# Performance work log

Measured on AMD Instinct MI355X. Metric: run time of the kernel, lower is better.

## Reference

```python
import jax, jax.numpy as jnp
import numpy as np

N_NODES = 50000
N_EDGES = 800000
D = 128          # node_state_dim
H = 256          # edge hidden / message dim (= 2*D)
NH = 256         # node MLP hidden


def setup_inputs() -> dict:
    key = jax.random.key(0)
    ks = jax.random.split(key, 20)
    s = 0.05
    inp = {
        "node_states": jax.random.normal(ks[0], (N_NODES, D), jnp.float32),
        "edge_features": jax.random.normal(ks[1], (N_EDGES, 1), jnp.float32),
        "from_idx": jax.random.randint(ks[2], (N_EDGES,), 0, N_NODES, jnp.int32),
        "to_idx": jax.random.randint(ks[3], (N_EDGES,), 0, N_NODES, jnp.int32),
        # forward-direction message net: Linear(2D+1 -> H), ReLU, Linear(H -> H)
        "W1": jax.random.normal(ks[4], (2 * D + 1, H), jnp.float32) * s,
        "b1": jnp.zeros((H,), jnp.float32),
        "W2": jax.random.normal(ks[5], (H, H), jnp.float32) * s,
        "b2": jnp.zeros((H,), jnp.float32),
        # reverse-direction message net (separate params)
        "RW1": jax.random.normal(ks[6], (2 * D + 1, H), jnp.float32) * s,
        "Rb1": jnp.zeros((H,), jnp.float32),
        "RW2": jax.random.normal(ks[7], (H, H), jnp.float32) * s,
        "Rb2": jnp.zeros((H,), jnp.float32),
        # node update MLP: Linear(3D -> NH), ReLU, Linear(NH -> D)
        "Wn1": jax.random.normal(ks[8], (3 * D, NH), jnp.float32) * s,
        "bn1": jnp.zeros((NH,), jnp.float32),
        "Wn2": jax.random.normal(ks[9], (NH, D), jnp.float32) * s,
        "bn2": jnp.zeros((D,), jnp.float32),
    }
    return inp


def _mlp2(x, W1, b1, W2, b2):
    return jax.nn.relu(x @ W1 + b1) @ W2 + b2


def reference(node_states, edge_features, from_idx, to_idx,
              W1, b1, W2, b2, RW1, Rb1, RW2, Rb2, Wn1, bn1, Wn2, bn2):
    n_nodes = node_states.shape[0]
    from_states = node_states[from_idx]            # [E, D]
    to_states = node_states[to_idx]                # [E, D]

    # forward direction: messages go to to_idx
    edge_in = jnp.concatenate([from_states, to_states, edge_features], axis=-1)  # [E, 2D+1]
    msgs = _mlp2(edge_in, W1, b1, W2, b2)                                        # [E, H]
    agg = jax.ops.segment_sum(msgs, to_idx, num_segments=n_nodes)                # [N, H]

    # reverse direction: swap roles, aggregate onto from_idx
    redge_in = jnp.concatenate([to_states, from_states, edge_features], axis=-1)
    rmsgs = _mlp2(redge_in, RW1, Rb1, RW2, Rb2)
    agg = agg + jax.ops.segment_sum(rmsgs, from_idx, num_segments=n_nodes)

    # residual node update: MLP on [agg, node_states] -> [N, D]
    upd_in = jnp.concatenate([agg, node_states], axis=-1)                        # [N, 3D]
    return node_states + _mlp2(upd_in, Wn1, bn1, Wn2, bn2)
```

## Files before the change

### kernel.cpp

```cpp
#include <hip/hip_runtime.h>
#include <hip/hip_bf16.h>


typedef __bf16 bf16;
typedef __attribute__((ext_vector_type(8))) __bf16 bf16x8;
typedef __attribute__((ext_vector_type(4))) __bf16 bf16x4v;
typedef __attribute__((ext_vector_type(4))) float floatx4;
typedef __attribute__((ext_vector_type(2))) float floatx2;

#define DD 128
#define HH 256
#define CAPB 1408
#define MAXBINS 1600

__device__ __forceinline__ bf16x8 ns8(const float* __restrict__ NS, int row, int col, int N) {
    bf16x8 v;
    if (row < N) {
        float4 f0 = *(const float4*)&NS[(size_t)row * DD + col];
        float4 f1 = *(const float4*)&NS[(size_t)row * DD + col + 4];
        v[0] = (bf16)f0.x; v[1] = (bf16)f0.y; v[2] = (bf16)f0.z; v[3] = (bf16)f0.w;
        v[4] = (bf16)f1.x; v[5] = (bf16)f1.y; v[6] = (bf16)f1.z; v[7] = (bf16)f1.w;
    } else {
        v = (bf16x8)(bf16)0.0f;
    }
    return v;
}

__global__ __launch_bounds__(256) void k_front(
    const float* __restrict__ NS, const int* __restrict__ from_idx,
    const int* __restrict__ to_idx, const float* __restrict__ ef,
    const float* __restrict__ W1, const float* __restrict__ RW1,
    const float* __restrict__ W2, const float* __restrict__ RW2,
    const float* __restrict__ Wn1, const float* __restrict__ Wn2,
    const float* __restrict__ b2, const float* __restrict__ Rb2,
    int* __restrict__ gcur, int2* __restrict__ binbuf,
    unsigned char* __restrict__ Pn, bf16* __restrict__ Pf,
    bf16* __restrict__ Wth, bf16* __restrict__ Wt2,
    float* __restrict__ u, float* __restrict__ ru,
    int E, int N, int NP, int NBINS, int BINB, int MB) {
    __shared__ __align__(16) unsigned char smem[20608];
    const int b = blockIdx.x, t = threadIdx.x;

    if (b < BINB) {
        int* hist = (int*)smem;
        int* base = hist + MAXBINS;
        const int NBF = NP >> 6;
        for (int i = t; i < NBINS; i += 256) hist[i] = 0;
        __syncthreads();
        const int e0 = b * 2048;
        int f[8], tt[8]; float w[8]; bool valid[8];
#pragma unroll
        for (int q = 0; q < 8; ++q) {
            int e = e0 + q * 256 + t;
            valid[q] = e < E;
            int ec = valid[q] ? e : 0;
            f[q] = from_idx[ec]; tt[q] = to_idx[ec]; w[q] = ef[ec];
        }
#pragma unroll
        for (int q = 0; q < 8; ++q) {
            if (valid[q]) {
                atomicAdd(&hist[tt[q] >> 6], 1);
                atomicAdd(&hist[NBF + (f[q] >> 6)], 1);
            }
        }
        __syncthreads();
        for (int i = t; i < NBINS; i += 256) {
            int h = hist[i];
            base[i] = h ? atomicAdd(&gcur[i], h) : 0;
            hist[i] = 0;
        }
        __syncthreads();
#pragma unroll
        for (int q = 0; q < 8; ++q) {
            if (valid[q]) {
                int wb = __float_as_int(w[q]);
                int b1 = tt[q] >> 6;
                int r1 = base[b1] + atomicAdd(&hist[b1], 1);
                if (r1 < CAPB)
                    binbuf[(size_t)b1 * CAPB + r1] = make_int2(((tt[q] & 63) << 17) | f[q], wb);
                int b2i = NBF + (f[q] >> 6);
                int r2 = base[b2i] + atomicAdd(&hist[b2i], 1);
                if (r2 < CAPB)
                    binbuf[(size_t)b2i * CAPB + r2] = make_int2(((f[q] & 63) << 17) | tt[q], wb);
            }
        }
        return;
    }

    if (b < BINB + 769) {
        int bb = b - BINB;
        if (bb < 640) {
            int k = bb, m = t;
            float v;
            if (k < 512) {
                const float* Wsrc = (k < 256) ? W2 : RW2;
                int i = k & 255;
                float acc = 0.f;
                for (int j = 0; j < 256; ++j) acc += Wsrc[i * 256 + j] * Wn1[j * 256 + m];
                v = acc;
            } else {
                v = Wn1[(256 + k - 512) * 256 + m];
            }
            Wth[m * 640 + k] = (bf16)v;
        } else if (bb < 768) {
            int idx = (bb - 640) * 256 + t;
            int n = idx >> 8, k = idx & 255;
            Wt2[idx] = (bf16)Wn2[k * 128 + n];
        } else {
            int m = t;
            float a = 0.f, c2 = 0.f;
            for (int j = 0; j < 256; ++j) {
                float w = Wn1[j * 256 + m];
                a += b2[j] * w;
                c2 += Rb2[j] * w;
            }
            u[m] = a;
            ru[m] = c2;
        }
        return;
    }

    {
        bf16 (*As)[64][40] = (bf16(*)[64][40])smem;
        bf16 (*Bs)[64][40] = (bf16(*)[64][40])(smem + 10240);
        const int p = b - (BINB + 769);
        const int col0 = (p / MB) * 64;
        const int row0 = (p % MB) * 64;
        const int wv = t >> 6, lane = t & 63;
        const int l15 = lane & 15, quad = lane >> 4;
        const int srow = t >> 2, kc = (t & 3) * 8;
        const int cb = col0 >> 8;
        const float* Wsrc = (cb < 2) ? W1 : RW1;
        const int krow_off = (cb & 1) ? 128 : 0;
        const int nb = col0 & 255;
        const int nloc = t & 63, kq = t >> 6;
        const int hB = kq >> 1, kk0 = (kq & 1) * 16;
        floatx4 acc[4] = {};
        for (int k0 = 0; k0 < DD; k0 += 64) {
            bf16x8 av0 = ns8(NS, row0 + srow, k0 + kc, N);
            bf16x8 av1 = ns8(NS, row0 + srow, k0 + 32 + kc, N);
            float bvals[16];
#pragma unroll
            for (int j = 0; j < 16; ++j)
                bvals[j] = Wsrc[(size_t)(krow_off + k0 + hB * 32 + kk0 + j) * 256 + nb + nloc];
            __syncthreads();
            *(bf16x8*)&As[0][srow][kc] = av0;
            *(bf16x8*)&As[1][srow][kc] = av1;
#pragma unroll
            for (int j = 0; j < 16; ++j)
                Bs[hB][nloc][kk0 + j] = (bf16)bvals[j];
            __syncthreads();
#pragma unroll
            for (int h = 0; h < 2; ++h) {
                bf16x8 bfr = *(const bf16x8*)&Bs[h][wv * 16 + l15][quad * 8];
#pragma unroll
                for (int r = 0; r < 4; ++r) {
                    bf16x8 afr = *(const bf16x8*)&As[h][r * 16 + l15][quad * 8];
                    acc[r] = __builtin_amdgcn_mfma_f32_16x16x32_bf16(afr, bfr, acc[r], 0, 0, 0);
                }
            }
        }
        const int ocol = col0 + wv * 16 + l15;
        const int ch = ocol & 255;
        const int half = (ocol >> 9) & 1;
        const bool isNbr = ((ocol >> 8) & 1) == 0;
#pragma unroll
        for (int r = 0; r < 4; ++r)
#pragma unroll
            for (int i = 0; i < 4; ++i) {
                int orow = row0 + r * 16 + quad * 4 + i;
                float v = acc[r][i];
                if (isNbr) {
                    int pk = __builtin_amdgcn_cvt_pk_fp8_f32(v, v, 0, false);
                    Pn[(size_t)orow * 512 + half * 256 + ch] = (unsigned char)(pk & 0xFF);
                } else {
                    Pf[(size_t)orow * 512 + half * 256 + ch] = (bf16)v;
                }
            }
    }
}

__global__ __launch_bounds__(256) void k_aggf(
    const unsigned char* __restrict__ Pn, const bf16* __restrict__ Pf,
    const int2* __restrict__ binbuf, const int* __restrict__ gcnt,
    const float* __restrict__ W1, const float* __restrict__ b1,
    const float* __restrict__ RW1, const float* __restrict__ Rb1,
    bf16* __restrict__ S_to, bf16* __restrict__ S_fr,
    int* __restrict__ deg, int NP) {
    __shared__ int hist[64], kstart[64], cur[64], scanbuf[64];
    __shared__ int2 srec[CAPB];
    const int b = blockIdx.x, t = threadIdx.x;
    const int NBF = NP >> 6;
    const bool rev = b >= NBF;
    const int node0 = (rev ? b - NBF : b) << 6;
    int cnt = gcnt[b]; if (cnt > CAPB) cnt = CAPB;
    const int2* bin = binbuf + (size_t)b * CAPB;
    if (t < 64) hist[t] = 0;
    __syncthreads();
    for (int i = t; i < cnt; i += 256)
        atomicAdd(&hist[((unsigned)bin[i].x) >> 17], 1);
    __syncthreads();
    if (t < 64) scanbuf[t] = hist[t];
    __syncthreads();
    for (int d = 1; d < 64; d <<= 1) {
        int v = (t < 64 && t >= d) ? scanbuf[t - d] : 0;
        __syncthreads();
        if (t < 64) scanbuf[t] += v;
        __syncthreads();
    }
    if (t < 64) { kstart[t] = scanbuf[t] - hist[t]; cur[t] = scanbuf[t] - hist[t]; }
    __syncthreads();
    for (int i = t; i < cnt; i += 256) {
        int2 r = bin[i];
        int rk = atomicAdd(&cur[((unsigned)r.x) >> 17], 1);
        srec[rk] = r;
    }
    __syncthreads();
    const int wv = t >> 6, lane = t & 63, c = lane * 4;
    const int fixoff = rev ? 256 : 0;
    const int nbroff = rev ? 256 : 0;
    const float* bb = rev ? Rb1 : b1;
    const float* wl = (rev ? RW1 : W1) + 65536;
    float4 bv = *(const float4*)&bb[c];
    float4 wv4 = *(const float4*)&wl[c];
    bf16* Sarr = rev ? S_fr : S_to;
    for (int key = wv; key < 64; key += 4) {
        int node = node0 + key;
        bf16x4v pf = *(const bf16x4v*)&Pf[(size_t)node * 512 + fixoff + c];
        float fx0 = (float)pf[0] + bv.x;
        float fx1 = (float)pf[1] + bv.y;
        float fx2 = (float)pf[2] + bv.z;
        float fx3 = (float)pf[3] + bv.w;
        int beg = kstart[key], kc2 = hist[key], end = beg + kc2;
        float a0 = 0.f, a1 = 0.f, a2 = 0.f, a3 = 0.f;
        int j = beg;
        for (; j + 8 <= end; j += 8) {
            int2 rr[8]; int qq[8];
#pragma unroll
            for (int z = 0; z < 8; ++z) rr[z] = srec[j + z];
#pragma unroll
            for (int z = 0; z < 8; ++z)
                qq[z] = *(const int*)&Pn[(size_t)(rr[z].x & 0x1FFFF) * 512 + nbroff + c];
#pragma unroll
            for (int z = 0; z < 8; ++z) {
                float w = __int_as_float(rr[z].y);
                floatx2 lo = __builtin_amdgcn_cvt_pk_f32_fp8(qq[z], false);
                floatx2 hi = __builtin_amdgcn_cvt_pk_f32_fp8(qq[z], true);
                a0 += fmaxf(fx0 + lo.x + w * wv4.x, 0.f);
                a1 += fmaxf(fx1 + lo.y + w * wv4.y, 0.f);
                a2 += fmaxf(fx2 + hi.x + w * wv4.z, 0.f);
                a3 += fmaxf(fx3 + hi.y + w * wv4.w, 0.f);
            }
        }
        for (; j < end; ++j) {
            int2 r = srec[j];
            int qq = *(const int*)&Pn[(size_t)(r.x & 0x1FFFF) * 512 + nbroff + c];
            float w = __int_as_float(r.y);
            floatx2 lo = __builtin_amdgcn_cvt_pk_f32_fp8(qq, false);
            floatx2 hi = __builtin_amdgcn_cvt_pk_f32_fp8(qq, true);
            a0 += fmaxf(fx0 + lo.x + w * wv4.x, 0.f);
            a1 += fmaxf(fx1 + lo.y + w * wv4.y, 0.f);
            a2 += fmaxf(fx2 + hi.x + w * wv4.z, 0.f);
            a3 += fmaxf(fx3 + hi.y + w * wv4.w, 0.f);
        }
        bf16x4v o;
        o[0] = (bf16)a0; o[1] = (bf16)a1; o[2] = (bf16)a2; o[3] = (bf16)a3;
        *(bf16x4v*)&Sarr[(size_t)node * 256 + c] = o;
        if (lane == 0) deg[(rev ? NP : 0) + node] = kc2;
    }
}

__global__ __launch_bounds__(256) void k_node(
    const bf16* __restrict__ S_to, const bf16* __restrict__ S_fr,
    const float* __restrict__ NS, const bf16* __restrict__ Wth,
    const bf16* __restrict__ Wt2,
    const float* __restrict__ u, const float* __restrict__ ru,
    const float* __restrict__ bn1, const float* __restrict__ bn2,
    const int* __restrict__ deg, float* __restrict__ out, int NP, int N) {
    __shared__ __align__(16) unsigned char smem[51200];
    bf16 (*As)[64][40]  = (bf16(*)[64][40])smem;
    bf16 (*Bs)[256][40] = (bf16(*)[256][40])(smem + 10240);
    bf16 (*Hs)[264] = (bf16(*)[264])smem;
    const int tid = threadIdx.x;
    const int wv = tid >> 6, lane = tid & 63;
    const int l15 = lane & 15, quad = lane >> 4;
    const int row0 = blockIdx.x * 64;
    const int srow4 = tid >> 2, kc = (tid & 3) * 8;
    floatx4 acc[4][4] = {};
    const int arow = row0 + srow4;
    auto loadA = [&](int k) -> bf16x8 {
        if (k < 512) {
            const bf16* S = (k < 256) ? S_to : S_fr;
            return *(const bf16x8*)&S[(size_t)arow * 256 + (k & 255) + kc];
        }
        return ns8(NS, arow, (k - 512) + kc, N);
    };
    for (int k0 = 0; k0 < 640; k0 += 64) {
        bf16x8 av0 = loadA(k0);
        bf16x8 av1 = loadA(k0 + 32);
        bf16x8 bv[2][4];
#pragma unroll
        for (int h = 0; h < 2; ++h)
#pragma unroll
            for (int j = 0; j < 4; ++j)
                bv[h][j] = *(const bf16x8*)&Wth[(size_t)(srow4 + 64 * j) * 640 + k0 + h * 32 + kc];
        __syncthreads();
        *(bf16x8*)&As[0][srow4][kc] = av0;
        *(bf16x8*)&As[1][srow4][kc] = av1;
#pragma unroll
        for (int h = 0; h < 2; ++h)
#pragma unroll
            for (int j = 0; j < 4; ++j)
                *(bf16x8*)&Bs[h][srow4 + 64 * j][kc] = bv[h][j];
        __syncthreads();
#pragma unroll
        for (int h = 0; h < 2; ++h)
#pragma unroll
            for (int s = 0; s < 4; ++s) {
                bf16x8 bfr = *(const bf16x8*)&Bs[h][wv * 64 + s * 16 + l15][quad * 8];
#pragma unroll
                for (int r = 0; r < 4; ++r) {
                    bf16x8 afr = *(const bf16x8*)&As[h][r * 16 + l15][quad * 8];
                    acc[s][r] = __builtin_amdgcn_mfma_f32_16x16x32_bf16(afr, bfr, acc[s][r], 0, 0, 0);
                }
            }
    }
    __syncthreads();
#pragma unroll
    for (int s = 0; s < 4; ++s) {
        int col = wv * 64 + s * 16 + l15;
        float uc = u[col], rc = ru[col], bc = bn1[col];
#pragma unroll
        for (int r = 0; r < 4; ++r)
#pragma unroll
            for (int i = 0; i < 4; ++i) {
                int row = r * 16 + quad * 4 + i;
                float v = acc[s][r][i] + (float)deg[row0 + row] * uc
                        + (float)deg[NP + row0 + row] * rc + bc;
                Hs[row][col] = (bf16)fmaxf(v, 0.f);
            }
    }
    __syncthreads();
    floatx4 acc2[2][4] = {};
    for (int k0 = 0; k0 < HH; k0 += 32) {
        bf16x8 afr[4];
#pragma unroll
        for (int r = 0; r < 4; ++r)
            afr[r] = *(const bf16x8*)&Hs[r * 16 + l15][k0 + quad * 8];
#pragma unroll
        for (int s = 0; s < 2; ++s) {
            int col = wv * 32 + s * 16 + l15;
            bf16x8 bfr = *(const bf16x8*)&Wt2[(size_t)col * HH + k0 + quad * 8];
#pragma unroll
            for (int r = 0; r < 4; ++r)
                acc2[s][r] = __builtin_amdgcn_mfma_f32_16x16x32_bf16(afr[r], bfr, acc2[s][r], 0, 0, 0);
        }
    }
#pragma unroll
    for (int s = 0; s < 2; ++s) {
        int ocol = wv * 32 + s * 16 + l15;
        float bb = bn2[ocol];
#pragma unroll
        for (int r = 0; r < 4; ++r)
#pragma unroll
            for (int i = 0; i < 4; ++i) {
                int orow = row0 + r * 16 + quad * 4 + i;
                if (orow < N)
                    out[(size_t)orow * DD + ocol] = acc2[s][r][i] + bb + NS[(size_t)orow * DD + ocol];
            }
    }
}

extern "C" void kernel_launch(void* const* d_in, const int* in_sizes, int n_in,
                              void* d_out, int out_size, void* d_ws, size_t ws_size,
                              hipStream_t stream) {
    const float* NS   = (const float*)d_in[0];
    const float* ef   = (const float*)d_in[1];
    const int* from_idx = (const int*)d_in[2];
    const int* to_idx   = (const int*)d_in[3];
    const float* W1  = (const float*)d_in[4];
    const float* b1  = (const float*)d_in[5];
    const float* W2  = (const float*)d_in[6];
    const float* b2  = (const float*)d_in[7];
    const float* RW1 = (const float*)d_in[8];
    const float* Rb1 = (const float*)d_in[9];
    const float* RW2 = (const float*)d_in[10];
    const float* Rb2 = (const float*)d_in[11];
    const float* Wn1 = (const float*)d_in[12];
    const float* bn1 = (const float*)d_in[13];
    const float* Wn2 = (const float*)d_in[14];
    const float* bn2 = (const float*)d_in[15];

    const int N  = in_sizes[0] / DD;
    const int E  = in_sizes[2];
    const int NP = ((N + 63) / 64) * 64;
    const int MB = NP / 64;
    const int NBF = NP / 64;
    const int NBINS = 2 * NBF;
    const int BINB = (E + 2047) / 2048;
    const int FRONT = BINB + 769 + 16 * MB;

    char* base = (char*)d_ws;
    size_t off_b = 0;
    auto alloc = [&](size_t b) { size_t o = off_b; off_b += (b + 255) & ~(size_t)255; return o; };
    unsigned char* Pn = (unsigned char*)(base + alloc((size_t)NP * 512));
    bf16* Pf   = (bf16*)(base + alloc((size_t)NP * 512 * 2));
    bf16* S_to = (bf16*)(base + alloc((size_t)NP * 256 * 2));
    bf16* S_fr = (bf16*)(base + alloc((size_t)NP * 256 * 2));
    int* deg   = (int*)(base + alloc((size_t)2 * NP * 4));
    int* gcur  = (int*)(base + alloc((size_t)NBINS * 4));
    int2* binbuf = (int2*)(base + alloc((size_t)NBINS * CAPB * 8));
    bf16* Wth = (bf16*)(base + alloc(256 * 640 * 2));
    bf16* Wt2 = (bf16*)(base + alloc(128 * 256 * 2));
    float* u  = (float*)(base + alloc(256 * 4));
    float* ru = (float*)(base + alloc(256 * 4));

    hipMemsetAsync(gcur, 0, (size_t)NBINS * 4, stream);

    k_front<<<FRONT, 256, 0, stream>>>(NS, from_idx, to_idx, ef,
                                       W1, RW1, W2, RW2, Wn1, Wn2, b2, Rb2,
                                       gcur, binbuf, Pn, Pf, Wth, Wt2, u, ru,
                                       E, N, NP, NBINS, BINB, MB);
    k_aggf<<<NBINS, 256, 0, stream>>>(Pn, Pf, binbuf, gcur, W1, b1, RW1, Rb1,
                                      S_to, S_fr, deg, NP);
    k_node<<<MB, 256, 0, stream>>>(S_to, S_fr, NS, Wth, Wt2, u, ru, bn1, bn2,
                                   deg, (float*)d_out, NP, N);
}
```

Measured before the change: 346.1 us.

## Halve aggregation bin size, pre-transpose W1 to bf16, replace memset with prep kernel

Shrinks the node bins in the edge binning and aggregation kernels from 64 to 32 nodes, doubling the bin count and aggregation blocks while cutting per-block shared memory and bin capacity. Adds a small prep kernel that writes W1/RW1 transposed to bf16 and zeroes the bin counters, replacing the memset. The front GEMM then loads B tiles as vectorized bf16 rows instead of strided fp32 scalar loads, and its tile order becomes row-major. Costs one extra launch, and the smaller bin capacity raises the risk of dropping edges when a bin overflows.

Measured after the change: 329.4 us. 4.8% less time.

```diff
diff --git a/kernel.cpp b/kernel.cpp
--- a/kernel.cpp
+++ b/kernel.cpp
@@ -10,8 +10,8 @@
 
 #define DD 128
 #define HH 256
-#define CAPB 1408
-#define MAXBINS 1600
+#define CAPB 800
+#define MAXBINS 3200
 
 __device__ __forceinline__ bf16x8 ns8(const float* __restrict__ NS, int row, int col, int N) {
     bf16x8 v;
@@ -26,25 +26,43 @@
     return v;
 }
 
+__global__ void k_pre(const float* __restrict__ W1, const float* __restrict__ RW1,
+                      bf16* __restrict__ Wt1, int* __restrict__ gcur, int NBINS) {
+    const int b = blockIdx.x, t = threadIdx.x;
+    if (b < 512) {
+        int idx = b * 256 + t;
+        int n = idx >> 7, k = idx & 127;
+        float v;
+        if (n < 256)      v = W1[k * 256 + n];
+        else if (n < 512) v = W1[(128 + k) * 256 + (n - 256)];
+        else if (n < 768) v = RW1[k * 256 + (n - 512)];
+        else              v = RW1[(128 + k) * 256 + (n - 768)];
+        Wt1[idx] = (bf16)v;
+    } else {
+        int i = (b - 512) * 256 + t;
+        if (i < NBINS) gcur[i] = 0;
+    }
+}
+
 __global__ __launch_bounds__(256) void k_front(
     const float* __restrict__ NS, const int* __restrict__ from_idx,
     const int* __restrict__ to_idx, const float* __restrict__ ef,
-    const float* __restrict__ W1, const float* __restrict__ RW1,
     const float* __restrict__ W2, const float* __restrict__ RW2,
     const float* __restrict__ Wn1, const float* __restrict__ Wn2,
     const float* __restrict__ b2, const float* __restrict__ Rb2,
+    const bf16* __restrict__ Wt1,
     int* __restrict__ gcur, int2* __restrict__ binbuf,
     unsigned char* __restrict__ Pn, bf16* __restrict__ Pf,
     bf16* __restrict__ Wth, bf16* __restrict__ Wt2,
     float* __restrict__ u, float* __restrict__ ru,
     int E, int N, int NP, int NBINS, int BINB, int MB) {
-    __shared__ __align__(16) unsigned char smem[20608];
+    __shared__ __align__(16) unsigned char smem[25600];
     const int b = blockIdx.x, t = threadIdx.x;
 
     if (b < BINB) {
         int* hist = (int*)smem;
         int* base = hist + MAXBINS;
-        const int NBF = NP >> 6;
+        const int NBF = NP >> 5;
         for (int i = t; i < NBINS; i += 256) hist[i] = 0;
         __syncthreads();
         const int e0 = b * 2048;
@@ -59,8 +77,8 @@
 #pragma unroll
         for (int q = 0; q < 8; ++q) {
             if (valid[q]) {
-                atomicAdd(&hist[tt[q] >> 6], 1);
-                atomicAdd(&hist[NBF + (f[q] >> 6)], 1);
+                atomicAdd(&hist[tt[q] >> 5], 1);
+                atomicAdd(&hist[NBF + (f[q] >> 5)], 1);
             }
         }
         __syncthreads();
@@ -74,14 +92,14 @@
         for (int q = 0; q < 8; ++q) {
             if (valid[q]) {
                 int wb = __float_as_int(w[q]);
-                int b1 = tt[q] >> 6;
+                int b1 = tt[q] >> 5;
                 int r1 = base[b1] + atomicAdd(&hist[b1], 1);
                 if (r1 < CAPB)
-                    binbuf[(size_t)b1 * CAPB + r1] = make_int2(((tt[q] & 63) << 17) | f[q], wb);
-                int b2i = NBF + (f[q] >> 6);
+                    binbuf[(size_t)b1 * CAPB + r1] = make_int2(((tt[q] & 31) << 17) | f[q], wb);
+                int b2i = NBF + (f[q] >> 5);
                 int r2 = base[b2i] + atomicAdd(&hist[b2i], 1);
                 if (r2 < CAPB)
-                    binbuf[(size_t)b2i * CAPB + r2] = make_int2(((f[q] & 63) << 17) | tt[q], wb);
+                    binbuf[(size_t)b2i * CAPB + r2] = make_int2(((f[q] & 31) << 17) | tt[q], wb);
             }
         }
         return;
@@ -124,31 +142,22 @@
         bf16 (*As)[64][40] = (bf16(*)[64][40])smem;
         bf16 (*Bs)[64][40] = (bf16(*)[64][40])(smem + 10240);
         const int p = b - (BINB + 769);
-        const int col0 = (p / MB) * 64;
-        const int row0 = (p % MB) * 64;
+        const int row0 = (p >> 4) * 64;
+        const int col0 = (p & 15) * 64;
         const int wv = t >> 6, lane = t & 63;
         const int l15 = lane & 15, quad = lane >> 4;
         const int srow = t >> 2, kc = (t & 3) * 8;
-        const int cb = col0 >> 8;
-        const float* Wsrc = (cb < 2) ? W1 : RW1;
-        const int krow_off = (cb & 1) ? 128 : 0;
-        const int nb = col0 & 255;
-        const int nloc = t & 63, kq = t >> 6;
-        const int hB = kq >> 1, kk0 = (kq & 1) * 16;
         floatx4 acc[4] = {};
         for (int k0 = 0; k0 < DD; k0 += 64) {
             bf16x8 av0 = ns8(NS, row0 + srow, k0 + kc, N);
             bf16x8 av1 = ns8(NS, row0 + srow, k0 + 32 + kc, N);
-            float bvals[16];
-#pragma unroll
-            for (int j = 0; j < 16; ++j)
-                bvals[j] = Wsrc[(size_t)(krow_off + k0 + hB * 32 + kk0 + j) * 256 + nb + nloc];
+            bf16x8 bv0 = *(const bf16x8*)&Wt1[(size_t)(col0 + srow) * DD + k0 + kc];
+            bf16x8 bv1 = *(const bf16x8*)&Wt1[(size_t)(col0 + srow) * DD + k0 + 32 + kc];
             __syncthreads();
             *(bf16x8*)&As[0][srow][kc] = av0;
             *(bf16x8*)&As[1][srow][kc] = av1;
-#pragma unroll
-            for (int j = 0; j < 16; ++j)
-                Bs[hB][nloc][kk0 + j] = (bf16)bvals[j];
+            *(bf16x8*)&Bs[0][srow][kc] = bv0;
+            *(bf16x8*)&Bs[1][srow][kc] = bv1;
             __syncthreads();
 #pragma unroll
             for (int h = 0; h < 2; ++h) {
@@ -187,28 +196,28 @@
     const float* __restrict__ RW1, const float* __restrict__ Rb1,
     bf16* __restrict__ S_to, bf16* __restrict__ S_fr,
     int* __restrict__ deg, int NP) {
-    __shared__ int hist[64], kstart[64], cur[64], scanbuf[64];
+    __shared__ int hist[32], kstart[32], cur[32], scanbuf[32];
     __shared__ int2 srec[CAPB];
     const int b = blockIdx.x, t = threadIdx.x;
-    const int NBF = NP >> 6;
+    const int NBF = NP >> 5;
     const bool rev = b >= NBF;
-    const int node0 = (rev ? b - NBF : b) << 6;
+    const int node0 = (rev ? b - NBF : b) << 5;
     int cnt = gcnt[b]; if (cnt > CAPB) cnt = CAPB;
     const int2* bin = binbuf + (size_t)b * CAPB;
-    if (t < 64) hist[t] = 0;
+    if (t < 32) hist[t] = 0;
     __syncthreads();
     for (int i = t; i < cnt; i += 256)
         atomicAdd(&hist[((unsigned)bin[i].x) >> 17], 1);
     __syncthreads();
-    if (t < 64) scanbuf[t] = hist[t];
-    __syncthreads();
-    for (int d = 1; d < 64; d <<= 1) {
-        int v = (t < 64 && t >= d) ? scanbuf[t - d] : 0;
-        __syncthreads();
-        if (t < 64) scanbuf[t] += v;
-        __syncthreads();
-    }
-    if (t < 64) { kstart[t] = scanbuf[t] - hist[t]; cur[t] = scanbuf[t] - hist[t]; }
+    if (t < 32) scanbuf[t] = hist[t];
+    __syncthreads();
+    for (int d = 1; d < 32; d <<= 1) {
+        int v = (t < 32 && t >= d) ? scanbuf[t - d] : 0;
+        __syncthreads();
+        if (t < 32) scanbuf[t] += v;
+        __syncthreads();
+    }
+    if (t < 32) { kstart[t] = scanbuf[t] - hist[t]; cur[t] = scanbuf[t] - hist[t]; }
     __syncthreads();
     for (int i = t; i < cnt; i += 256) {
         int2 r = bin[i];
@@ -224,7 +233,7 @@
     float4 bv = *(const float4*)&bb[c];
     float4 wv4 = *(const float4*)&wl[c];
     bf16* Sarr = rev ? S_fr : S_to;
-    for (int key = wv; key < 64; key += 4) {
+    for (int key = wv; key < 32; key += 4) {
         int node = node0 + key;
         bf16x4v pf = *(const bf16x4v*)&Pf[(size_t)node * 512 + fixoff + c];
         float fx0 = (float)pf[0] + bv.x;
@@ -395,10 +404,11 @@
     const int E  = in_sizes[2];
     const int NP = ((N + 63) / 64) * 64;
     const int MB = NP / 64;
-    const int NBF = NP / 64;
+    const int NBF = NP / 32;
     const int NBINS = 2 * NBF;
     const int BINB = (E + 2047) / 2048;
     const int FRONT = BINB + 769 + 16 * MB;
+    const int PREB = 512 + (NBINS + 255) / 256;
 
     char* base = (char*)d_ws;
     size_t off_b = 0;
@@ -410,15 +420,15 @@
     int* deg   = (int*)(base + alloc((size_t)2 * NP * 4));
     int* gcur  = (int*)(base + alloc((size_t)NBINS * 4));
     int2* binbuf = (int2*)(base + alloc((size_t)NBINS * CAPB * 8));
+    bf16* Wt1 = (bf16*)(base + alloc(1024 * 128 * 2));
     bf16* Wth = (bf16*)(base + alloc(256 * 640 * 2));
     bf16* Wt2 = (bf16*)(base + alloc(128 * 256 * 2));
     float* u  = (float*)(base + alloc(256 * 4));
     float* ru = (float*)(base + alloc(256 * 4));
 
-    hipMemsetAsync(gcur, 0, (size_t)NBINS * 4, stream);
-
+    k_pre<<<PREB, 256, 0, stream>>>(W1, RW1, Wt1, gcur, NBINS);
     k_front<<<FRONT, 256, 0, stream>>>(NS, from_idx, to_idx, ef,
-                                       W1, RW1, W2, RW2, Wn1, Wn2, b2, Rb2,
+                                       W2, RW2, Wn1, Wn2, b2, Rb2, Wt1,
                                        gcur, binbuf, Pn, Pf, Wth, Wt2, u, ru,
                                        E, N, NP, NBINS, BINB, MB);
     k_aggf<<<NBINS, 256, 0, stream>>>(Pn, Pf, binbuf, gcur, W1, b1, RW1, Rb1,
```
